# Kernel tuning notes

Hardware: AMD Instinct MI355X
Metric: run time of the kernel (lower is better)

The kernel has to match this reference:

```python
import jax, jax.numpy as jnp
import numpy as np

B, L, H, E = 4, 2048, 8, 64

def setup_inputs() -> dict:
    key = jax.random.key(0)
    kq, kk, kv = jax.random.split(key, 3)
    queries = jax.random.normal(kq, (B, L, H, E), dtype=jnp.float32)
    keys = jax.random.normal(kk, (B, L, H, E), dtype=jnp.float32)
    values = jax.random.normal(kv, (B, L, H, E), dtype=jnp.float32)
    return {"queries": queries, "keys": keys, "values": values}

def reference(queries, keys, values):
    # queries/keys/values: [B, L, H, E]
    E_ = queries.shape[-1]
    scale = 1.0 / jnp.sqrt(jnp.float32(E_))
    # scores: [B, H, L, S]
    scores = jnp.einsum('blhe,bshe->bhls', queries, keys)
    Lq, S = scores.shape[-2], scores.shape[-1]
    # TriangularCausalMask: mask positions where s > l (strict upper triangle)
    causal = jnp.tril(jnp.ones((Lq, S), dtype=bool))
    scores = jnp.where(causal, scores, -jnp.inf)
    A = jax.nn.softmax(scale * scores, axis=-1)  # dropout p=0 -> identity
    V = jnp.einsum('bhls,bshd->blhd', A, values)
    return V
```

## Files before the change

kernel.cpp:

```cpp
#include <hip/hip_runtime.h>


#define Bc 4
#define Lc 2048
#define Hc 8
#define Ec 64
#define KVT 64
#define NKV (Lc / KVT)
#define TILEB 8192
#define BHB ((size_t)NKV * TILEB)
#define WSV ((size_t)32 * BHB)

using f32x4 = __attribute__((ext_vector_type(4))) float;
using f16x8 = __attribute__((ext_vector_type(8))) _Float16;
using f16x4 = __attribute__((ext_vector_type(4))) _Float16;
using hf16x2 = __fp16 __attribute__((ext_vector_type(2)));

static __device__ __forceinline__ unsigned int pk2(float lo, float hi) {
    union { hf16x2 h; unsigned int u; } c;
    c.h = __builtin_amdgcn_cvt_pkrtz(lo, hi);
    return c.u;
}

__global__ __launch_bounds__(256)
void prep_kernel(const float* __restrict__ K, const float* __restrict__ V,
                 char* __restrict__ ws)
{
    __shared__ char kst[64 * 128];
    __shared__ char vst[64 * 144];
    __shared__ char vtt[64 * 128];

    const int bid = blockIdx.x;
    const int bh = bid >> 5, kt = bid & 31;
    const int b = bh >> 3, h = bh & 7;
    const int tid = threadIdx.x;
    const size_t base = (size_t)b * Lc * Hc * Ec + (size_t)h * Ec;

    {
        const int r = tid >> 2, q4 = tid & 3, c0 = 16 * q4;
        const float* kp = K + base + (size_t)(kt * 64 + r) * 512 + c0;
        const float* vp = V + base + (size_t)(kt * 64 + r) * 512 + c0;
        unsigned int wk[8], wv[8];
        #pragma unroll
        for (int i = 0; i < 4; ++i) {
            float4 fk = *(const float4*)(kp + 4 * i);
            float4 fv = *(const float4*)(vp + 4 * i);
            wk[2*i]   = pk2(fk.x, fk.y); wk[2*i+1] = pk2(fk.z, fk.w);
            wv[2*i]   = pk2(fv.x, fv.y); wv[2*i+1] = pk2(fv.z, fv.w);
        }
        *(uint4*)(kst + r * 128 + 2 * c0)      = *(uint4*)&wk[0];
        *(uint4*)(kst + r * 128 + 2 * c0 + 16) = *(uint4*)&wk[4];
        *(uint4*)(vst + r * 144 + 2 * c0)      = *(uint4*)&wv[0];
        *(uint4*)(vst + r * 144 + 2 * c0 + 16) = *(uint4*)&wv[4];
    }
    __syncthreads();
    {
        const int e = tid >> 2, kq = tid & 3, kv0 = 16 * kq;
        unsigned int w[8];
        #pragma unroll
        for (int i = 0; i < 8; ++i) {
            unsigned int lo = *(const unsigned short*)(vst + (kv0 + 2*i)     * 144 + 2*e);
            unsigned int hi = *(const unsigned short*)(vst + (kv0 + 2*i + 1) * 144 + 2*e);
            w[i] = lo | (hi << 16);
        }
        *(uint4*)(vtt + e * 128 + 2 * kv0)      = *(uint4*)&w[0];
        *(uint4*)(vtt + e * 128 + 2 * kv0 + 16) = *(uint4*)&w[4];
    }
    __syncthreads();
    {
        const int lane = tid & 63, qq = tid >> 6;
        const int l15 = lane & 15, l4 = lane >> 4;
        char* ko = ws + (size_t)bh * BHB + (size_t)kt * TILEB;
        char* vo = ws + WSV + (size_t)bh * BHB + (size_t)kt * TILEB;
        uint4 k0 = *(const uint4*)(kst + (16 * qq + l15) * 128 + 16 * l4);
        uint4 k1 = *(const uint4*)(kst + (16 * qq + l15) * 128 + 64 + 16 * l4);
        *(uint4*)(ko + (2 * qq)     * 1024 + lane * 16) = k0;
        *(uint4*)(ko + (2 * qq + 1) * 1024 + lane * 16) = k1;
        unsigned long long vv[4];
        #pragma unroll
        for (int c = 0; c < 4; ++c)
            vv[c] = *(const unsigned long long*)(vtt + (16 * c + l15) * 128 + 32 * qq + 8 * l4);
        uint4 v01, v23;
        v01.x = (unsigned)vv[0]; v01.y = (unsigned)(vv[0] >> 32);
        v01.z = (unsigned)vv[1]; v01.w = (unsigned)(vv[1] >> 32);
        v23.x = (unsigned)vv[2]; v23.y = (unsigned)(vv[2] >> 32);
        v23.z = (unsigned)vv[3]; v23.w = (unsigned)(vv[3] >> 32);
        *(uint4*)(vo + (2 * qq)     * 1024 + lane * 16) = v01;
        *(uint4*)(vo + (2 * qq + 1) * 1024 + lane * 16) = v23;
    }
}

__global__ __launch_bounds__(64, 2)
void fa_fwd_kernel(const float* __restrict__ Q, const char* __restrict__ ws,
                   float* __restrict__ Out)
{
    const int bid = blockIdx.x;
    const int xcd = bid & 7;
    const int rr  = bid >> 3;
    const int bh  = 4 * xcd + (rr & 3);
    const int qi  = rr >> 2;
    const int qt  = 63 - qi;
    const int steps = (qt >> 1) + 1;
    const int b = bh >> 3, h = bh & 7;

    const int lane = threadIdx.x;
    const int l15 = lane & 15, l4 = lane >> 4;
    const size_t base = (size_t)b * Lc * Hc * Ec + (size_t)h * Ec;
    const char* kimg = ws + (size_t)bh * BHB + lane * 16;
    const char* vimg = ws + WSV + (size_t)bh * BHB + lane * 16;
    const float SL2E = 0.125f * 1.44269504088896340736f;

    f16x4 ones;
    {
        const _Float16 ov = (_Float16)((l15 == 0) ? 1.0f : 0.0f);
        ones[0] = ov; ones[1] = ov; ones[2] = ov; ones[3] = ov;
    }

    f16x8 qa[2][2];
    #pragma unroll
    for (int g = 0; g < 2; ++g) {
        const int qrow = qt * 32 + 16 * g + l15;
        const float* qpr = Q + base + (size_t)qrow * 512 + 8 * l4;
        float4 f0 = *(const float4*)(qpr);
        float4 f1 = *(const float4*)(qpr + 4);
        float4 f2 = *(const float4*)(qpr + 32);
        float4 f3 = *(const float4*)(qpr + 36);
        union { f16x8 v; unsigned int u[4]; } pk;
        pk.u[0] = pk2(f0.x * SL2E, f0.y * SL2E);
        pk.u[1] = pk2(f0.z * SL2E, f0.w * SL2E);
        pk.u[2] = pk2(f1.x * SL2E, f1.y * SL2E);
        pk.u[3] = pk2(f1.z * SL2E, f1.w * SL2E);
        qa[g][0] = pk.v;
        pk.u[0] = pk2(f2.x * SL2E, f2.y * SL2E);
        pk.u[1] = pk2(f2.z * SL2E, f2.w * SL2E);
        pk.u[2] = pk2(f3.x * SL2E, f3.y * SL2E);
        pk.u[3] = pk2(f3.z * SL2E, f3.w * SL2E);
        qa[g][1] = pk.v;
    }

    f32x4 o[2][4] = {};
    f32x4 ol[2] = {};
    float m_run[2] = {-1e30f, -1e30f};

    uint4 kf[8], vf[8];
    #pragma unroll
    for (int j = 0; j < 8; ++j) kf[j] = *(const uint4*)(kimg + j * 1024);
    #pragma unroll
    for (int j = 0; j < 8; ++j) vf[j] = *(const uint4*)(vimg + j * 1024);

    #pragma unroll 1
    for (int kt = 0; kt < steps; ++kt) {
        f32x4 s[2][4];
        #pragma unroll
        for (int n = 0; n < 4; ++n) {
            union { uint4 u; f16x8 h; } a0, a1;
            a0.u = kf[2 * n]; a1.u = kf[2 * n + 1];
            #pragma unroll
            for (int g = 0; g < 2; ++g) {
                f32x4 z = {0.f, 0.f, 0.f, 0.f};
                z = __builtin_amdgcn_mfma_f32_16x16x32_f16(a0.h, qa[g][0], z, 0, 0, 0);
                z = __builtin_amdgcn_mfma_f32_16x16x32_f16(a1.h, qa[g][1], z, 0, 0, 0);
                s[g][n] = z;
            }
        }

        if (kt + 1 < steps) {
            const char* kp = kimg + (size_t)(kt + 1) * TILEB;
            #pragma unroll
            for (int j = 0; j < 8; ++j) kf[j] = *(const uint4*)(kp + j * 1024);
        }

        if (kt == steps - 1) {
            #pragma unroll
            for (int g = 0; g < 2; ++g) {
                const int q_g = qt * 32 + 16 * g + l15;
                #pragma unroll
                for (int n = 0; n < 4; ++n) {
                    #pragma unroll
                    for (int r2 = 0; r2 < 4; ++r2) {
                        const int kv_g = kt * 64 + 16 * n + 4 * l4 + r2;
                        if (kv_g > q_g) s[g][n][r2] = -1e30f;
                    }
                }
            }
        }

        float pmax[2];
        #pragma unroll
        for (int g = 0; g < 2; ++g) {
            float a0 = fmaxf(s[g][0][0], s[g][0][1]), a1 = fmaxf(s[g][0][2], s[g][0][3]);
            float a2 = fmaxf(s[g][1][0], s[g][1][1]), a3 = fmaxf(s[g][1][2], s[g][1][3]);
            float a4 = fmaxf(s[g][2][0], s[g][2][1]), a5 = fmaxf(s[g][2][2], s[g][2][3]);
            float a6 = fmaxf(s[g][3][0], s[g][3][1]), a7 = fmaxf(s[g][3][2], s[g][3][3]);
            float pm = fmaxf(fmaxf(fmaxf(a0, a1), fmaxf(a2, a3)),
                             fmaxf(fmaxf(a4, a5), fmaxf(a6, a7)));
            pm = fmaxf(pm, __shfl_xor(pm, 16, 64));
            pm = fmaxf(pm, __shfl_xor(pm, 32, 64));
            pmax[g] = pm;
        }
        #pragma unroll
        for (int g = 0; g < 2; ++g) {
            if (!__all(pmax[g] - m_run[g] <= 8.0f)) {
                const float m_new = fmaxf(m_run[g], pmax[g]);
                const float fac = __builtin_exp2f(m_run[g] - m_new);
                m_run[g] = m_new;
                float fr[4];
                #pragma unroll
                for (int r2 = 0; r2 < 4; ++r2) fr[r2] = __shfl(fac, 4 * l4 + r2, 64);
                #pragma unroll
                for (int c = 0; c < 4; ++c)
                    #pragma unroll
                    for (int r2 = 0; r2 < 4; ++r2) o[g][c][r2] *= fr[r2];
                #pragma unroll
                for (int r2 = 0; r2 < 4; ++r2) ol[g][r2] *= fr[r2];
            }
        }

        unsigned int ph[2][4][2];
        #pragma unroll
        for (int g = 0; g < 2; ++g) {
            #pragma unroll
            for (int n = 0; n < 4; ++n) {
                float p0 = __builtin_exp2f(s[g][n][0] - m_run[g]);
                float p1 = __builtin_exp2f(s[g][n][1] - m_run[g]);
                float p2 = __builtin_exp2f(s[g][n][2] - m_run[g]);
                float p3 = __builtin_exp2f(s[g][n][3] - m_run[g]);
                ph[g][n][0] = pk2(p0, p1);
                ph[g][n][1] = pk2(p2, p3);
            }
        }

        #pragma unroll
        for (int m = 0; m < 4; ++m) {
            union { uint4 u; f16x4 h[2]; } w0, w1;
            w0.u = vf[2 * m]; w1.u = vf[2 * m + 1];
            #pragma unroll
            for (int g = 0; g < 2; ++g) {
                union { f16x4 h; unsigned int u[2]; } pa;
                pa.u[0] = ph[g][m][0]; pa.u[1] = ph[g][m][1];
                ol[g] = __builtin_amdgcn_mfma_f32_16x16x16f16(pa.h, ones, ol[g], 0, 0, 0);
                o[g][0] = __builtin_amdgcn_mfma_f32_16x16x16f16(pa.h, w0.h[0], o[g][0], 0, 0, 0);
                o[g][1] = __builtin_amdgcn_mfma_f32_16x16x16f16(pa.h, w0.h[1], o[g][1], 0, 0, 0);
                o[g][2] = __builtin_amdgcn_mfma_f32_16x16x16f16(pa.h, w1.h[0], o[g][2], 0, 0, 0);
                o[g][3] = __builtin_amdgcn_mfma_f32_16x16x16f16(pa.h, w1.h[1], o[g][3], 0, 0, 0);
            }
        }

        if (kt + 1 < steps) {
            const char* vp2 = vimg + (size_t)(kt + 1) * TILEB;
            #pragma unroll
            for (int j = 0; j < 8; ++j) vf[j] = *(const uint4*)(vp2 + j * 1024);
        }
    }

    float* op = Out + base;
    #pragma unroll
    for (int g = 0; g < 2; ++g) {
        float ir[4];
        #pragma unroll
        for (int r2 = 0; r2 < 4; ++r2) {
            const float iv = 1.0f / ol[g][r2];
            ir[r2] = __shfl(iv, 16 * l4, 64);
        }
        const int qrow0 = qt * 32 + 16 * g;
        #pragma unroll
        for (int c = 0; c < 4; ++c)
            #pragma unroll
            for (int r2 = 0; r2 < 4; ++r2)
                op[(size_t)(qrow0 + 4 * l4 + r2) * 512 + 16 * c + l15] = o[g][c][r2] * ir[r2];
    }
}

extern "C" void kernel_launch(void* const* d_in, const int* in_sizes, int n_in,
                              void* d_out, int out_size, void* d_ws, size_t ws_size,
                              hipStream_t stream) {
    const float* Q = (const float*)d_in[0];
    const float* K = (const float*)d_in[1];
    const float* V = (const float*)d_in[2];
    float* O = (float*)d_out;
    char* ws = (char*)d_ws;
    hipLaunchKernelGGL(prep_kernel, dim3(32 * NKV), dim3(256), 0, stream, K, V, ws);
    hipLaunchKernelGGL(fa_fwd_kernel, dim3(2048), dim3(64), 0, stream, Q, ws, O);
}
```

Baseline: 60.92 us.

## Restructure attention into 8-wave blocks with paired causal query tiles

The forward kernel moves from 2048 single-wave blocks, each handling 32 query rows, to 256 blocks of 8 waves. Each wave owns 16 query rows, and each block processes two 128-row query tiles (p and 15-p) so causal work is balanced across blocks. Each wave streams its own K/V copy from the workspace, which relies on L2 reuse across the waves in a block, and the XCD-aware block mapping is dropped. Nontemporal loads for Q/K/V and nontemporal output stores are added to reduce cache pollution.

```diff
diff --git a/kernel.cpp b/kernel.cpp
--- a/kernel.cpp
+++ b/kernel.cpp
@@ -5,9 +5,8 @@
 #define Lc 2048
 #define Hc 8
 #define Ec 64
-#define KVT 64
-#define NKV (Lc / KVT)
 #define TILEB 8192
+#define NKV 32
 #define BHB ((size_t)NKV * TILEB)
 #define WSV ((size_t)32 * BHB)
 
@@ -15,11 +14,15 @@
 using f16x8 = __attribute__((ext_vector_type(8))) _Float16;
 using f16x4 = __attribute__((ext_vector_type(4))) _Float16;
 using hf16x2 = __fp16 __attribute__((ext_vector_type(2)));
+using u32x4 = __attribute__((ext_vector_type(4))) unsigned int;
 
 static __device__ __forceinline__ unsigned int pk2(float lo, float hi) {
     union { hf16x2 h; unsigned int u; } c;
     c.h = __builtin_amdgcn_cvt_pkrtz(lo, hi);
     return c.u;
+}
+static __device__ __forceinline__ u32x4 nt16(const void* p) {
+    return __builtin_nontemporal_load((const u32x4*)p);
 }
 
 __global__ __launch_bounds__(256)
@@ -43,10 +46,11 @@
         unsigned int wk[8], wv[8];
         #pragma unroll
         for (int i = 0; i < 4; ++i) {
-            float4 fk = *(const float4*)(kp + 4 * i);
-            float4 fv = *(const float4*)(vp + 4 * i);
-            wk[2*i]   = pk2(fk.x, fk.y); wk[2*i+1] = pk2(fk.z, fk.w);
-            wv[2*i]   = pk2(fv.x, fv.y); wv[2*i+1] = pk2(fv.z, fv.w);
+            union { u32x4 v; float f[4]; } fk, fv;
+            fk.v = nt16(kp + 4 * i);
+            fv.v = nt16(vp + 4 * i);
+            wk[2*i]   = pk2(fk.f[0], fk.f[1]); wk[2*i+1] = pk2(fk.f[2], fk.f[3]);
+            wv[2*i]   = pk2(fv.f[0], fv.f[1]); wv[2*i+1] = pk2(fv.f[2], fv.f[3]);
         }
         *(uint4*)(kst + r * 128 + 2 * c0)      = *(uint4*)&wk[0];
         *(uint4*)(kst + r * 128 + 2 * c0 + 16) = *(uint4*)&wk[4];
@@ -90,21 +94,20 @@
     }
 }
 
-__global__ __launch_bounds__(64, 2)
+__global__ __launch_bounds__(512, 2)
 void fa_fwd_kernel(const float* __restrict__ Q, const char* __restrict__ ws,
                    float* __restrict__ Out)
 {
     const int bid = blockIdx.x;
-    const int xcd = bid & 7;
-    const int rr  = bid >> 3;
-    const int bh  = 4 * xcd + (rr & 3);
-    const int qi  = rr >> 2;
-    const int qt  = 63 - qi;
-    const int steps = (qt >> 1) + 1;
-    const int b = bh >> 3, h = bh & 7;
-
-    const int lane = threadIdx.x;
-    const int l15 = lane & 15, l4 = lane >> 4;
+    const int bh  = bid & 31;
+    const int p   = bid >> 5;
+    const int b   = bh >> 3, h = bh & 7;
+
+    const int tid  = threadIdx.x;
+    const int wid  = tid >> 6;
+    const int lane = tid & 63;
+    const int l15  = lane & 15, l4 = lane >> 4;
+
     const size_t base = (size_t)b * Lc * Hc * Ec + (size_t)h * Ec;
     const char* kimg = ws + (size_t)bh * BHB + lane * 16;
     const char* vimg = ws + WSV + (size_t)bh * BHB + lane * 16;
@@ -116,158 +119,140 @@
         ones[0] = ov; ones[1] = ov; ones[2] = ov; ones[3] = ov;
     }
 
-    f16x8 qa[2][2];
-    #pragma unroll
-    for (int g = 0; g < 2; ++g) {
-        const int qrow = qt * 32 + 16 * g + l15;
-        const float* qpr = Q + base + (size_t)qrow * 512 + 8 * l4;
-        float4 f0 = *(const float4*)(qpr);
-        float4 f1 = *(const float4*)(qpr + 4);
-        float4 f2 = *(const float4*)(qpr + 32);
-        float4 f3 = *(const float4*)(qpr + 36);
-        union { f16x8 v; unsigned int u[4]; } pk;
-        pk.u[0] = pk2(f0.x * SL2E, f0.y * SL2E);
-        pk.u[1] = pk2(f0.z * SL2E, f0.w * SL2E);
-        pk.u[2] = pk2(f1.x * SL2E, f1.y * SL2E);
-        pk.u[3] = pk2(f1.z * SL2E, f1.w * SL2E);
-        qa[g][0] = pk.v;
-        pk.u[0] = pk2(f2.x * SL2E, f2.y * SL2E);
-        pk.u[1] = pk2(f2.z * SL2E, f2.w * SL2E);
-        pk.u[2] = pk2(f3.x * SL2E, f3.y * SL2E);
-        pk.u[3] = pk2(f3.z * SL2E, f3.w * SL2E);
-        qa[g][1] = pk.v;
-    }
-
-    f32x4 o[2][4] = {};
-    f32x4 ol[2] = {};
-    float m_run[2] = {-1e30f, -1e30f};
-
-    uint4 kf[8], vf[8];
-    #pragma unroll
-    for (int j = 0; j < 8; ++j) kf[j] = *(const uint4*)(kimg + j * 1024);
-    #pragma unroll
-    for (int j = 0; j < 8; ++j) vf[j] = *(const uint4*)(vimg + j * 1024);
-
     #pragma unroll 1
-    for (int kt = 0; kt < steps; ++kt) {
-        f32x4 s[2][4];
-        #pragma unroll
-        for (int n = 0; n < 4; ++n) {
-            union { uint4 u; f16x8 h; } a0, a1;
-            a0.u = kf[2 * n]; a1.u = kf[2 * n + 1];
-            #pragma unroll
-            for (int g = 0; g < 2; ++g) {
+    for (int half = 0; half < 2; ++half) {
+        const int qt = half ? p : (15 - p);
+        const int qrow0 = qt * 128 + 16 * wid;
+        const int mysteps = 2 * qt + 1 + (wid >> 2);
+
+        f16x8 qa0, qa1;
+        {
+            const float* qpr = Q + base + (size_t)(qrow0 + l15) * 512 + 8 * l4;
+            union { u32x4 v; float f[4]; } f0, f1, f2, f3;
+            f0.v = nt16(qpr);      f1.v = nt16(qpr + 4);
+            f2.v = nt16(qpr + 32); f3.v = nt16(qpr + 36);
+            union { f16x8 v; unsigned int u[4]; } pk;
+            pk.u[0] = pk2(f0.f[0] * SL2E, f0.f[1] * SL2E);
+            pk.u[1] = pk2(f0.f[2] * SL2E, f0.f[3] * SL2E);
+            pk.u[2] = pk2(f1.f[0] * SL2E, f1.f[1] * SL2E);
+            pk.u[3] = pk2(f1.f[2] * SL2E, f1.f[3] * SL2E);
+            qa0 = pk.v;
+            pk.u[0] = pk2(f2.f[0] * SL2E, f2.f[1] * SL2E);
+            pk.u[1] = pk2(f2.f[2] * SL2E, f2.f[3] * SL2E);
+            pk.u[2] = pk2(f3.f[0] * SL2E, f3.f[1] * SL2E);
+            pk.u[3] = pk2(f3.f[2] * SL2E, f3.f[3] * SL2E);
+            qa1 = pk.v;
+        }
+
+        f32x4 o[4] = {};
+        f32x4 ol = {};
+        float m_run = -1e30f;
+
+        uint4 kf[8], vf[8];
+        #pragma unroll
+        for (int j = 0; j < 8; ++j) kf[j] = *(const uint4*)(kimg + j * 1024);
+        #pragma unroll
+        for (int j = 0; j < 8; ++j) vf[j] = *(const uint4*)(vimg + j * 1024);
+
+        #pragma unroll 1
+        for (int kt = 0; kt < mysteps; ++kt) {
+            f32x4 s[4];
+            #pragma unroll
+            for (int n = 0; n < 4; ++n) {
+                union { uint4 u; f16x8 h; } a0, a1;
+                a0.u = kf[2 * n]; a1.u = kf[2 * n + 1];
                 f32x4 z = {0.f, 0.f, 0.f, 0.f};
-                z = __builtin_amdgcn_mfma_f32_16x16x32_f16(a0.h, qa[g][0], z, 0, 0, 0);
-                z = __builtin_amdgcn_mfma_f32_16x16x32_f16(a1.h, qa[g][1], z, 0, 0, 0);
-                s[g][n] = z;
-            }
-        }
-
-        if (kt + 1 < steps) {
-            const char* kp = kimg + (size_t)(kt + 1) * TILEB;
-            #pragma unroll
-            for (int j = 0; j < 8; ++j) kf[j] = *(const uint4*)(kp + j * 1024);
-        }
-
-        if (kt == steps - 1) {
-            #pragma unroll
-            for (int g = 0; g < 2; ++g) {
-                const int q_g = qt * 32 + 16 * g + l15;
+                z = __builtin_amdgcn_mfma_f32_16x16x32_f16(a0.h, qa0, z, 0, 0, 0);
+                z = __builtin_amdgcn_mfma_f32_16x16x32_f16(a1.h, qa1, z, 0, 0, 0);
+                s[n] = z;
+            }
+
+            if (kt + 1 < mysteps) {
+                const char* kp = kimg + (size_t)(kt + 1) * TILEB;
+                #pragma unroll
+                for (int j = 0; j < 8; ++j) kf[j] = *(const uint4*)(kp + j * 1024);
+            }
+
+            if (kt == mysteps - 1) {
+                const int q_g = qrow0 + l15;
                 #pragma unroll
                 for (int n = 0; n < 4; ++n) {
                     #pragma unroll
                     for (int r2 = 0; r2 < 4; ++r2) {
                         const int kv_g = kt * 64 + 16 * n + 4 * l4 + r2;
-                        if (kv_g > q_g) s[g][n][r2] = -1e30f;
+                        if (kv_g > q_g) s[n][r2] = -1e30f;
                     }
                 }
             }
-        }
-
-        float pmax[2];
-        #pragma unroll
-        for (int g = 0; g < 2; ++g) {
-            float a0 = fmaxf(s[g][0][0], s[g][0][1]), a1 = fmaxf(s[g][0][2], s[g][0][3]);
-            float a2 = fmaxf(s[g][1][0], s[g][1][1]), a3 = fmaxf(s[g][1][2], s[g][1][3]);
-            float a4 = fmaxf(s[g][2][0], s[g][2][1]), a5 = fmaxf(s[g][2][2], s[g][2][3]);
-            float a6 = fmaxf(s[g][3][0], s[g][3][1]), a7 = fmaxf(s[g][3][2], s[g][3][3]);
-            float pm = fmaxf(fmaxf(fmaxf(a0, a1), fmaxf(a2, a3)),
-                             fmaxf(fmaxf(a4, a5), fmaxf(a6, a7)));
-            pm = fmaxf(pm, __shfl_xor(pm, 16, 64));
-            pm = fmaxf(pm, __shfl_xor(pm, 32, 64));
-            pmax[g] = pm;
-        }
-        #pragma unroll
-        for (int g = 0; g < 2; ++g) {
-            if (!__all(pmax[g] - m_run[g] <= 8.0f)) {
-                const float m_new = fmaxf(m_run[g], pmax[g]);
-                const float fac = __builtin_exp2f(m_run[g] - m_new);
-                m_run[g] = m_new;
+
+            float a0 = fmaxf(s[0][0], s[0][1]), a1 = fmaxf(s[0][2], s[0][3]);
+            float a2 = fmaxf(s[1][0], s[1][1]), a3 = fmaxf(s[1][2], s[1][3]);
+            float a4 = fmaxf(s[2][0], s[2][1]), a5 = fmaxf(s[2][2], s[2][3]);
+            float a6 = fmaxf(s[3][0], s[3][1]), a7 = fmaxf(s[3][2], s[3][3]);
+            float pmax = fmaxf(fmaxf(fmaxf(a0, a1), fmaxf(a2, a3)),
+                               fmaxf(fmaxf(a4, a5), fmaxf(a6, a7)));
+            pmax = fmaxf(pmax, __shfl_xor(pmax, 16, 64));
+            pmax = fmaxf(pmax, __shfl_xor(pmax, 32, 64));
+
+            if (!__all(pmax - m_run <= 8.0f)) {
+                const float m_new = fmaxf(m_run, pmax);
+                const float fac = __builtin_exp2f(m_run - m_new);
+                m_run = m_new;
                 float fr[4];
                 #pragma unroll
                 for (int r2 = 0; r2 < 4; ++r2) fr[r2] = __shfl(fac, 4 * l4 + r2, 64);
                 #pragma unroll
                 for (int c = 0; c < 4; ++c)
                     #pragma unroll
-                    for (int r2 = 0; r2 < 4; ++r2) o[g][c][r2] *= fr[r2];
-                #pragma unroll
-                for (int r2 = 0; r2 < 4; ++r2) ol[g][r2] *= fr[r2];
-            }
-        }
-
-        unsigned int ph[2][4][2];
-        #pragma unroll
-        for (int g = 0; g < 2; ++g) {
+                    for (int r2 = 0; r2 < 4; ++r2) o[c][r2] *= fr[r2];
+                #pragma unroll
+                for (int r2 = 0; r2 < 4; ++r2) ol[r2] *= fr[r2];
+            }
+
+            unsigned int ph[4][2];
             #pragma unroll
             for (int n = 0; n < 4; ++n) {
-                float p0 = __builtin_exp2f(s[g][n][0] - m_run[g]);
-                float p1 = __builtin_exp2f(s[g][n][1] - m_run[g]);
-                float p2 = __builtin_exp2f(s[g][n][2] - m_run[g]);
-                float p3 = __builtin_exp2f(s[g][n][3] - m_run[g]);
-                ph[g][n][0] = pk2(p0, p1);
-                ph[g][n][1] = pk2(p2, p3);
-            }
-        }
-
-        #pragma unroll
-        for (int m = 0; m < 4; ++m) {
-            union { uint4 u; f16x4 h[2]; } w0, w1;
-            w0.u = vf[2 * m]; w1.u = vf[2 * m + 1];
-            #pragma unroll
-            for (int g = 0; g < 2; ++g) {
+                float p0 = __builtin_exp2f(s[n][0] - m_run);
+                float p1 = __builtin_exp2f(s[n][1] - m_run);
+                float p2 = __builtin_exp2f(s[n][2] - m_run);
+                float p3 = __builtin_exp2f(s[n][3] - m_run);
+                ph[n][0] = pk2(p0, p1);
+                ph[n][1] = pk2(p2, p3);
+            }
+
+            #pragma unroll
+            for (int m = 0; m < 4; ++m) {
+                union { uint4 u; f16x4 h[2]; } w0, w1;
+                w0.u = vf[2 * m]; w1.u = vf[2 * m + 1];
                 union { f16x4 h; unsigned int u[2]; } pa;
-                pa.u[0] = ph[g][m][0]; pa.u[1] = ph[g][m][1];
-                ol[g] = __builtin_amdgcn_mfma_f32_16x16x16f16(pa.h, ones, ol[g], 0, 0, 0);
-                o[g][0] = __builtin_amdgcn_mfma_f32_16x16x16f16(pa.h, w0.h[0], o[g][0], 0, 0, 0);
-                o[g][1] = __builtin_amdgcn_mfma_f32_16x16x16f16(pa.h, w0.h[1], o[g][1], 0, 0, 0);
-                o[g][2] = __builtin_amdgcn_mfma_f32_16x16x16f16(pa.h, w1.h[0], o[g][2], 0, 0, 0);
-                o[g][3] = __builtin_amdgcn_mfma_f32_16x16x16f16(pa.h, w1.h[1], o[g][3], 0, 0, 0);
-            }
-        }
-
-        if (kt + 1 < steps) {
-            const char* vp2 = vimg + (size_t)(kt + 1) * TILEB;
-            #pragma unroll
-            for (int j = 0; j < 8; ++j) vf[j] = *(const uint4*)(vp2 + j * 1024);
-        }
-    }
-
-    float* op = Out + base;
-    #pragma unroll
-    for (int g = 0; g < 2; ++g) {
+                pa.u[0] = ph[m][0]; pa.u[1] = ph[m][1];
+                ol   = __builtin_amdgcn_mfma_f32_16x16x16f16(pa.h, ones,    ol,   0, 0, 0);
+                o[0] = __builtin_amdgcn_mfma_f32_16x16x16f16(pa.h, w0.h[0], o[0], 0, 0, 0);
+                o[1] = __builtin_amdgcn_mfma_f32_16x16x16f16(pa.h, w0.h[1], o[1], 0, 0, 0);
+                o[2] = __builtin_amdgcn_mfma_f32_16x16x16f16(pa.h, w1.h[0], o[2], 0, 0, 0);
+                o[3] = __builtin_amdgcn_mfma_f32_16x16x16f16(pa.h, w1.h[1], o[3], 0, 0, 0);
+            }
+
+            if (kt + 1 < mysteps) {
+                const char* vp2 = vimg + (size_t)(kt + 1) * TILEB;
+                #pragma unroll
+                for (int j = 0; j < 8; ++j) vf[j] = *(const uint4*)(vp2 + j * 1024);
+            }
+        }
+
         float ir[4];
         #pragma unroll
         for (int r2 = 0; r2 < 4; ++r2) {
-            const float iv = 1.0f / ol[g][r2];
+            const float iv = 1.0f / ol[r2];
             ir[r2] = __shfl(iv, 16 * l4, 64);
         }
-        const int qrow0 = qt * 32 + 16 * g;
+        float* op = Out + base;
         #pragma unroll
         for (int c = 0; c < 4; ++c)
             #pragma unroll
             for (int r2 = 0; r2 < 4; ++r2)
-                op[(size_t)(qrow0 + 4 * l4 + r2) * 512 + 16 * c + l15] = o[g][c][r2] * ir[r2];
+                __builtin_nontemporal_store(o[c][r2] * ir[r2],
+                    op + (size_t)(qrow0 + 4 * l4 + r2) * 512 + 16 * c + l15);
     }
 }
 
@@ -280,5 +265,5 @@
     float* O = (float*)d_out;
     char* ws = (char*)d_ws;
     hipLaunchKernelGGL(prep_kernel, dim3(32 * NKV), dim3(256), 0, stream, K, V, ws);
-    hipLaunchKernelGGL(fa_fwd_kernel, dim3(2048), dim3(64), 0, stream, Q, ws, O);
-}
+    hipLaunchKernelGGL(fa_fwd_kernel, dim3(256), dim3(512), 0, stream, Q, ws, O);
+}
```

After: 70.15 us. 15.1% more time.
